# Performance work log

Hardware: AMD Instinct MI355X
Metric: run time of the kernel (lower is better)

## Reference

```python
import jax, jax.numpy as jnp
import numpy as np
from jax import lax

FEAT_X, FEAT_Y = 50, 37          # generate_anchors(50, 37)
BASE_SIZE, DSR = 8.0, 16.0
A = FEAT_X * FEAT_Y * 9          # 16650 anchors


def generate_anchors():
    # Vectorized version of the triple python loop; order: x, y, size, [b1,b2,b3]
    xs = jnp.arange(FEAT_X, dtype=jnp.float32)[:, None, None]
    ys = jnp.arange(FEAT_Y, dtype=jnp.float32)[None, :, None]
    s = jnp.array([BASE_SIZE, 2 * BASE_SIZE, 4 * BASE_SIZE], jnp.float32)[None, None, :]

    def box(x1, y1, x2, y2):
        return jnp.stack(jnp.broadcast_arrays(x1 * DSR, y1 * DSR, x2 * DSR, y2 * DSR), axis=-1)

    b1 = box(xs - s / 2, ys - s / 2, xs + s / 2, ys + s / 2)      # square
    b2 = box(xs - s,     ys - s / 4, xs + s,     ys + s / 4)      # wide
    b3 = box(xs - s / 4, ys - s,     xs + s / 4, ys + s)          # tall
    anchors = jnp.stack([b1, b2, b3], axis=3)  # (50,37,3 sizes,3 variants,4)
    return anchors.reshape(-1, 4)              # (16650,4)


def conv2d(x, w, b, padding):
    y = lax.conv_general_dilated(x, w, (1, 1), padding,
                                 dimension_numbers=("NCHW", "OIHW", "NCHW"))
    return y + b[None, :, None, None]


def pairwise_iou(anchors, gt):
    # anchors: (A,4), gt: (B,G,4) -> iou (B,A,G); zero when no positive overlap
    a = anchors[None, :, None, :]
    g = gt[:, None, :, :]
    area_a = (a[..., 2] - a[..., 0]) * (a[..., 3] - a[..., 1])
    area_g = (g[..., 2] - g[..., 0]) * (g[..., 3] - g[..., 1])
    left = jnp.maximum(a[..., 0], g[..., 0])
    right = jnp.minimum(a[..., 2], g[..., 2])
    top = jnp.maximum(a[..., 1], g[..., 1])
    bot = jnp.minimum(a[..., 3], g[..., 3])
    no_ov = (left >= right) | (top >= bot)
    inter = jnp.where(no_ov, 0.0, (right - left) * (bot - top))
    return jnp.where(no_ov, 0.0, inter / (area_a + area_g - inter))


def setup_inputs() -> dict:
    key = jax.random.key(0)
    k1, k2, k3, k4, k5, k6, k7, k8 = jax.random.split(key, 8)
    B, G = 8, 20
    feats = jax.random.normal(k1, (B, 512, FEAT_Y, FEAT_X), jnp.float32)
    # well-formed gt boxes inside an ~800x592 image
    raw = jax.random.uniform(k2, (B, G, 2, 2)) * jnp.array([800.0, 592.0])
    x1y1 = jnp.min(raw, axis=2)
    x2y2 = jnp.max(raw, axis=2) + 1.0
    gt_boxes = jnp.concatenate([x1y1, x2y2], axis=-1)  # (B,G,4)
    im_info = jnp.array([[592.0, 800.0, 1.0]], jnp.float32)  # (h, w, scale)
    s = 0.02
    w3 = jax.random.normal(k3, (512, 512, 3, 3), jnp.float32) * s
    b3 = jnp.zeros((512,), jnp.float32)
    wc = jax.random.normal(k4, (18, 512, 1, 1), jnp.float32) * s
    bc = jnp.zeros((18,), jnp.float32)
    wb = jax.random.normal(k5, (36, 512, 1, 1), jnp.float32) * s
    bb = jnp.zeros((36,), jnp.float32)
    return {"feats": feats, "w3": w3, "b3": b3, "wc": wc, "bc": bc,
            "wb": wb, "bb": bb, "gt_boxes": gt_boxes, "im_info": im_info}


def reference(feats, w3, b3, wc, bc, wb, bb, gt_boxes, im_info):
    B = feats.shape[0]
    anchors = generate_anchors()
    rpn_conv1 = jax.nn.relu(conv2d(feats, w3, b3, ((1, 1), (1, 1))))
    rpn_cls_score = conv2d(rpn_conv1, wc, bc, ((0, 0), (0, 0)))  # (B,18,H,W)
    Bc, C, H, W = rpn_cls_score.shape
    score_rs = rpn_cls_score.reshape(Bc, 2, (C * H) // 2, W)      # reshape(x, 2)
    rpn_cls_prob = jax.nn.softmax(score_rs, axis=1).reshape(Bc, 18, H, W)
    rpn_bbox_pred = conv2d(rpn_conv1, wb, bb, ((0, 0), (0, 0)))   # (B,36,H,W)

    # anchor-target assignment (training branch), faithful to original logic
    inside = ((anchors[:, 0] >= 0) & (anchors[:, 1] >= 0) &
              (anchors[:, 2] < im_info[0, 1]) & (anchors[:, 3] < im_info[0, 0]))
    iou = pairwise_iou(anchors, gt_boxes)                 # (B,A,G)
    iou = jnp.where(inside[None, :, None], iou, 0.0)      # outside anchors skipped
    G = gt_boxes.shape[1]
    # original: idxs = argmax(iou_matrix[:][j]) with j == last gt index
    idx = jnp.argmax(iou[:, G - 1, :], axis=-1)           # (B,)
    labels = jnp.zeros((B, anchors.shape[0]), jnp.float32)
    labels = labels.at[jnp.arange(B), idx].set(1.0)
    max_iou = jnp.max(iou, axis=-1)                       # (B,A)
    labels = jnp.where(inside[None, :] & (max_iou > 0.7), 0.0, labels)

    out = jnp.concatenate([rpn_cls_prob, rpn_bbox_pred], axis=1)  # (B,54,H,W)
    return out, iou, labels
```

## Files before the change

### kernel.cpp

```cpp
#include <hip/hip_runtime.h>

typedef unsigned short u16;
typedef unsigned int u32;
typedef float f32x4 __attribute__((ext_vector_type(4)));
typedef short bf16x8 __attribute__((ext_vector_type(8)));

#define NB 8
#define FH 37
#define FW 50
#define FHW 1850
#define MTOT 14800
#define CIN 512
#define KTOT 4608
#define HP 39
#define WP 52
#define ANCH 16650
#define NG 20
#define MPAD 14848
#define PSTRIDE 7602176

#define ZB 356
#define WTB 512
#define WHB 128
#define TRB 7424
#define PRE_TOT (ZB + WTB + WHB + TRB)

#define CONVB 1856
#define IOB 528

__device__ __forceinline__ u16 f2bf(float f) {
    u32 u = __float_as_uint(f);
    u += 0x7fffu + ((u >> 16) & 1u);
    return (u16)(u >> 16);
}

__device__ __forceinline__ void gl2lds16(const u16* g, u16* l) {
    __builtin_amdgcn_global_load_lds((const __attribute__((address_space(1))) void*)(g),
                                     (__attribute__((address_space(3))) void*)(l),
                                     16, 0, 0);
}

__device__ __forceinline__ void anchor_box(int a, float& x1, float& y1, float& x2, float& y2) {
    int x = a / 333;
    int rem = a - x * 333;
    int y = rem / 9;
    int r2 = rem - y * 9;
    int si = r2 / 3;
    int bi = r2 - si * 3;
    float s = (float)(8 << si);
    float fx = (float)x, fy = (float)y;
    float ax1, ay1, ax2, ay2;
    if (bi == 0)      { float h = s * 0.5f;  ax1 = fx - h; ay1 = fy - h; ax2 = fx + h; ay2 = fy + h; }
    else if (bi == 1) { float q = s * 0.25f; ax1 = fx - s; ay1 = fy - q; ax2 = fx + s; ay2 = fy + q; }
    else              { float q = s * 0.25f; ax1 = fx - q; ay1 = fy - s; ax2 = fx + q; ay2 = fy + s; }
    x1 = ax1 * 16.f; y1 = ay1 * 16.f; x2 = ax2 * 16.f; y2 = ay2 * 16.f;
}

__global__ __launch_bounds__(256) void k_pre(u16* __restrict__ apad,
                                             const float* __restrict__ w3, u16* __restrict__ wt,
                                             const float* __restrict__ wc, const float* __restrict__ wb,
                                             u16* __restrict__ whd,
                                             const float* __restrict__ feats) {
    __shared__ __attribute__((aligned(16))) char smraw[18432];
    int blk = blockIdx.x;
    int t = threadIdx.x;

    if (blk < ZB) {
        uint4* apad4 = (uint4*)apad;
        int i = blk * 256 + t;
        int img = i / 11392;
        int r = i - img * 11392;
        int u4;
        if (r < 3328) u4 = r;
        else if (r < 6656) u4 = 126464 + (r - 3328);
        else {
            int rp = r - 6656;
            int h = 1 + (rp >> 7);
            int c2 = rp & 127;
            int col = (c2 & 64) ? 51 : 0;
            u4 = (h * 52 + col) * 64 + (c2 & 63);
        }
        apad4[img * 129792 + u4] = make_uint4(0u, 0u, 0u, 0u);
    } else if (blk < ZB + WTB) {
        float* lt = (float*)smraw;
        int n = blk - ZB;
        const float* src = w3 + n * KTOT;
        for (int i = t; i < KTOT; i += 256) lt[i] = src[i];
        __syncthreads();
        u16* dst = wt + n * KTOT;
        for (int o = t; o < KTOT; o += 256) {
            int tap = o >> 9, ci = o & 511;
            dst[o] = f2bf(lt[ci * 9 + tap]);
        }
    } else if (blk < ZB + WTB + WHB) {
        int i = (blk - ZB - WTB) * 256 + t;
        int n = i >> 9;
        int ci = i & 511;
        float v = 0.f;
        if (n < 18) v = wc[n * 512 + ci];
        else if (n < 54) v = wb[(n - 18) * 512 + ci];
        whd[i] = f2bf(v);
    } else {
        float* tile = (float*)smraw;
        int q = blk - ZB - WTB - WHB;
        int xt = q % 58;
        int r2 = q / 58;
        int ct = r2 & 15;
        int img = r2 >> 4;
        int hw0 = xt * 32, c0 = ct * 32;
        int tx = t & 31, ty4 = t >> 5;
        #pragma unroll
        for (int rr = 0; rr < 4; rr++) {
            int ty = ty4 + rr * 8;
            int hw = hw0 + tx;
            if (hw < FHW) tile[ty * 33 + tx] = feats[(img * 512 + c0 + ty) * FHW + hw];
        }
        __syncthreads();
        #pragma unroll
        for (int rr = 0; rr < 4; rr++) {
            int ty = ty4 + rr * 8;
            int hw2 = hw0 + ty;
            if (hw2 < FHW) {
                int h = hw2 / FW, w = hw2 - h * FW;
                apad[(((img * HP) + h + 1) * WP + (w + 1)) * 512 + c0 + tx] = f2bf(tile[tx * 33 + ty]);
            }
        }
    }
}

__global__ __launch_bounds__(256) void k_conv(const u16* __restrict__ apad,
                                              const u16* __restrict__ wt,
                                              float* __restrict__ P,
                                              const float* __restrict__ gt,
                                              const float* __restrict__ im,
                                              float* __restrict__ iou_out,
                                              float* __restrict__ lab) {
    __shared__ __attribute__((aligned(16))) char sm[24576];
    __shared__ int idxs;
    int L = blockIdx.x;
    int tid = threadIdx.x;

    if (L < CONVB) {
        u16* As = (u16*)sm;
        u16* Bs = (u16*)(sm + 16384);
        int g = L >> 6;
        int pair = (L & 7) + 8 * g;
        int nb = (L >> 3) & 7;
        int mb = pair >> 1;
        int kh = pair & 1;
        int wave = tid >> 6, lane = tid & 63;
        int m0 = mb * 128;
        int n0 = nb * 64;
        int wr = wave >> 1, wn = wave & 1;
        int lm = lane & 15, lq = lane >> 4;
        int l7 = lm & 7;

        f32x4 acc[4][2] = {};

        int rloc = tid >> 3;
        int cg = (tid & 7) ^ (rloc & 7);
        int aBase[4], bBase[2];
        for (int i = 0; i < 4; i++) {
            int m = m0 + i * 32 + rloc; if (m > MTOT - 1) m = MTOT - 1;
            int b = m / FHW; int hw = m - b * FHW;
            int h = hw / FW; int w = hw - h * FW;
            aBase[i] = ((b * HP + h) * WP + w) * 512 + cg * 8;
        }
        for (int j = 0; j < 2; j++)
            bBase[j] = (n0 + j * 32 + rloc) * KTOT + cg * 8;

        u16* aL[4]; u16* bL[2];
        for (int i = 0; i < 4; i++) aL[i] = &As[(i * 32 + wave * 8) * 64];
        for (int j = 0; j < 2; j++) bL[j] = &Bs[(j * 32 + wave * 8) * 64];

        int kEnd = (kh + 1) * 2304;
        for (int kk = kh * 2304; kk < kEnd; kk += 64) {
            int tap = kk >> 9;
            int ci0 = kk & 511;
            int dy = tap / 3, dx = tap - dy * 3;
            int aOfs = (dy * WP + dx) * 512 + ci0;
            gl2lds16(apad + aBase[0] + aOfs, aL[0]);
            gl2lds16(apad + aBase[1] + aOfs, aL[1]);
            gl2lds16(apad + aBase[2] + aOfs, aL[2]);
            gl2lds16(apad + aBase[3] + aOfs, aL[3]);
            gl2lds16(wt + bBase[0] + kk, bL[0]);
            gl2lds16(wt + bBase[1] + kk, bL[1]);
            __syncthreads();
            bf16x8 a[2][4], b[2][2];
            #pragma unroll
            for (int ks = 0; ks < 2; ks++) {
                int slotb = ((ks * 4 + lq) ^ l7) * 8;
                #pragma unroll
                for (int i = 0; i < 4; i++)
                    a[ks][i] = *(const bf16x8*)&As[(wr * 64 + i * 16 + lm) * 64 + slotb];
                #pragma unroll
                for (int j = 0; j < 2; j++)
                    b[ks][j] = *(const bf16x8*)&Bs[(wn * 32 + j * 16 + lm) * 64 + slotb];
            }
            #pragma unroll
            for (int ks = 0; ks < 2; ks++)
                #pragma unroll
                for (int i = 0; i < 4; i++)
                    #pragma unroll
                    for (int j = 0; j < 2; j++)
                        acc[i][j] = __builtin_amdgcn_mfma_f32_16x16x32_bf16(a[ks][i], b[ks][j], acc[i][j], 0, 0, 0);
            __syncthreads();
        }

        float* Pp = P + (size_t)kh * PSTRIDE;
        for (int j = 0; j < 2; j++) {
            int n = n0 + wn * 32 + j * 16 + lm;
            for (int i = 0; i < 4; i++) {
                int mb2 = m0 + wr * 64 + i * 16 + lq * 4;
                for (int r = 0; r < 4; r++) {
                    int m = mb2 + r;
                    if (m < MTOT) Pp[m * 512 + n] = acc[i][j][r];
                }
            }
        }
    } else {
        float* g4 = (float*)sm;
        float* imv = g4 + 80;
        float* buf = g4 + 84;
        int q = L - CONVB;
        int at = q % 66;
        int b = q / 66;
        int t = tid;
        if (t < NG * 4) g4[t] = gt[b * NG * 4 + t];
        if (t < 2) imv[t] = im[t];
        __syncthreads();
        if (t == 0) {
            float x1, y1, x2, y2;
            anchor_box(19, x1, y1, x2, y2);
            bool inside = (x1 >= 0.f) && (y1 >= 0.f) && (x2 < imv[1]) && (y2 < imv[0]);
            float aa = (x2 - x1) * (y2 - y1);
            float best = -1.f; int bg = 0;
            for (int g2 = 0; g2 < NG; g2++) {
                float gx1 = g4[g2 * 4], gy1 = g4[g2 * 4 + 1], gx2 = g4[g2 * 4 + 2], gy2 = g4[g2 * 4 + 3];
                float l = fmaxf(x1, gx1), r = fminf(x2, gx2);
                float tp = fmaxf(y1, gy1), bo = fminf(y2, gy2);
                float v = 0.f;
                if (l < r && tp < bo) {
                    float inter = (r - l) * (bo - tp);
                    float ag = (gx2 - gx1) * (gy2 - gy1);
                    v = inter / (aa + ag - inter);
                }
                if (!inside) v = 0.f;
                if (v > best) { best = v; bg = g2; }
            }
            idxs = bg;
        }
        int a0 = at * 256;
        int a = a0 + t;
        float mx = 0.f;
        bool inside = false;
        if (a < ANCH) {
            float x1, y1, x2, y2;
            anchor_box(a, x1, y1, x2, y2);
            inside = (x1 >= 0.f) && (y1 >= 0.f) && (x2 < imv[1]) && (y2 < imv[0]);
            float aa = (x2 - x1) * (y2 - y1);
            for (int g2 = 0; g2 < NG; g2++) {
                float gx1 = g4[g2 * 4], gy1 = g4[g2 * 4 + 1], gx2 = g4[g2 * 4 + 2], gy2 = g4[g2 * 4 + 3];
                float l = fmaxf(x1, gx1), r = fminf(x2, gx2);
                float tp = fmaxf(y1, gy1), bo = fminf(y2, gy2);
                float v = 0.f;
                if (l < r && tp < bo) {
                    float inter = (r - l) * (bo - tp);
                    float ag = (gx2 - gx1) * (gy2 - gy1);
                    v = inter / (aa + ag - inter);
                }
                if (!inside) v = 0.f;
                buf[t * NG + g2] = v;
                mx = fmaxf(mx, v);
            }
        }
        __syncthreads();
        int rem = ANCH - a0;
        int cnt = (rem < 256 ? rem : 256) * NG;
        float* dst = iou_out + (b * ANCH + a0) * NG;
        for (int i = t; i < cnt; i += 256) dst[i] = buf[i];
        if (a < ANCH) {
            float lv = (a == idxs) ? 1.f : 0.f;
            if (inside && mx > 0.7f) lv = 0.f;
            lab[b * ANCH + a] = lv;
        }
    }
}

__global__ __launch_bounds__(256) void k_post(const float* __restrict__ P,
                                              const u16* __restrict__ whd,
                                              const float* __restrict__ b3,
                                              const float* __restrict__ bc,
                                              const float* __restrict__ bb,
                                              float* __restrict__ out) {
    __shared__ __attribute__((aligned(16))) u16 actT[32 * 64 * 8];
    __shared__ float Sl[4][16][68];
    int t = threadIdx.x;
    int m0 = blockIdx.x * 32;
    const float* P0 = P;
    const float* P1 = P + PSTRIDE;

    #pragma unroll
    for (int i = 0; i < 16; i++) {
        int idx = t + i * 256;
        int row = idx >> 7, col4 = idx & 127;
        size_t off = (size_t)(m0 + row) * 512 + col4 * 4;
        f32x4 p0 = *(const f32x4*)&P0[off];
        f32x4 p1 = *(const f32x4*)&P1[off];
        f32x4 bi = *(const f32x4*)&b3[col4 * 4];
        u32 lo, hi;
        {
            float v0 = p0[0] + p1[0] + bi[0]; v0 = v0 > 0.f ? v0 : 0.f;
            float v1 = p0[1] + p1[1] + bi[1]; v1 = v1 > 0.f ? v1 : 0.f;
            float v2 = p0[2] + p1[2] + bi[2]; v2 = v2 > 0.f ? v2 : 0.f;
            float v3 = p0[3] + p1[3] + bi[3]; v3 = v3 > 0.f ? v3 : 0.f;
            lo = (u32)f2bf(v0) | ((u32)f2bf(v1) << 16);
            hi = (u32)f2bf(v2) | ((u32)f2bf(v3) << 16);
        }
        int slot = row * 64 + ((col4 >> 1) ^ (row & 7));
        *(uint2*)&actT[slot * 8 + (col4 & 1) * 4] = make_uint2(lo, hi);
    }
    __syncthreads();

    int wave = t >> 6, lane = t & 63, lm = lane & 15, lq = lane >> 4;
    int g = wave >> 1, kh = wave & 1;
    int rowLoc = g * 16 + lm;
    f32x4 acc[4] = {};
    #pragma unroll
    for (int s = 0; s < 8; s++) {
        int kk = kh * 256 + s * 32;
        int c = (kk >> 3) + lq;
        bf16x8 a = *(const bf16x8*)&actT[(rowLoc * 64 + (c ^ (rowLoc & 7))) * 8];
        #pragma unroll
        for (int j = 0; j < 4; j++) {
            bf16x8 b = *(const bf16x8*)&whd[(j * 16 + lm) * 512 + kk + lq * 8];
            acc[j] = __builtin_amdgcn_mfma_f32_16x16x32_bf16(a, b, acc[j], 0, 0, 0);
        }
    }
    #pragma unroll
    for (int r = 0; r < 4; r++)
        #pragma unroll
        for (int j = 0; j < 4; j++)
            Sl[wave][lq * 4 + r][j * 16 + lm] = acc[j][r];
    __syncthreads();

    for (int i = t; i < 32 * 54; i += 256) {
        int row = i & 31, cc = i >> 5;
        int m = m0 + row;
        if (m >= MTOT) continue;
        int g2 = (row >> 4) * 2, rl = row & 15;
        float v;
        if (cc < 18) {
            int c0 = cc < 9 ? cc : cc - 9;
            float s0 = Sl[g2][rl][c0] + Sl[g2 + 1][rl][c0] + bc[c0];
            float s1 = Sl[g2][rl][c0 + 9] + Sl[g2 + 1][rl][c0 + 9] + bc[c0 + 9];
            float mx = fmaxf(s0, s1);
            float e0 = __expf(s0 - mx), e1 = __expf(s1 - mx);
            v = (cc < 9 ? e0 : e1) / (e0 + e1);
        } else {
            v = Sl[g2][rl][cc] + Sl[g2 + 1][rl][cc] + bb[cc - 18];
        }
        int b = m / FHW, hw = m - b * FHW;
        out[(b * 54 + cc) * FHW + hw] = v;
    }
}

extern "C" void kernel_launch(void* const* d_in, const int* in_sizes, int n_in,
                              void* d_out, int out_size, void* d_ws, size_t ws_size,
                              hipStream_t stream) {
    (void)in_sizes; (void)n_in; (void)out_size; (void)ws_size;
    const float* feats = (const float*)d_in[0];
    const float* w3    = (const float*)d_in[1];
    const float* b3    = (const float*)d_in[2];
    const float* wc    = (const float*)d_in[3];
    const float* bc    = (const float*)d_in[4];
    const float* wb    = (const float*)d_in[5];
    const float* bb    = (const float*)d_in[6];
    const float* gt    = (const float*)d_in[7];
    const float* im    = (const float*)d_in[8];
    float* out = (float*)d_out;
    char* ws = (char*)d_ws;

    u16* apad = (u16*)(ws);
    u16* wt   = (u16*)(ws + 16613376);
    u16* whd  = (u16*)(ws + 21331968);
    float* P  = (float*)(ws + 21397504);

    float* iou_out = out + 799200;
    float* lab     = out + 3463200;

    k_pre<<<dim3(PRE_TOT), dim3(256), 0, stream>>>(apad, w3, wt, wc, wb, whd, feats);
    k_conv<<<dim3(CONVB + IOB), dim3(256), 0, stream>>>(apad, wt, P, gt, im, iou_out, lab);
    k_post<<<dim3(464), dim3(256), 0, stream>>>(P, whd, b3, bc, bb, out);
}
```

Before: 206.8 us.

## Drop split-K and fuse bias/ReLU/heads into conv via last-block atomic counter

The 3x3 conv no longer splits K into two halves with fp32 partial outputs. Each block runs the full K loop and writes bias+ReLU activations directly as bf16. A per-M-tile atomic counter lets the last of the 8 N-blocks compute the 1x1 cls/bbox heads and softmax inline, which removes the separate post kernel and the fp32 partial round trip. The cost is half as many conv blocks, each with a longer serial K loop, so less parallelism. The tail work is also serialized on one block per M tile, and correctness depends on fences and the counter reset done in k_pre.

After: 367.7 us. +77.8%, slower.

```diff
diff --git a/kernel.cpp b/kernel.cpp
--- a/kernel.cpp
+++ b/kernel.cpp
@@ -16,8 +16,6 @@
 #define WP 52
 #define ANCH 16650
 #define NG 20
-#define MPAD 14848
-#define PSTRIDE 7602176
 
 #define ZB 356
 #define WTB 512
@@ -25,7 +23,7 @@
 #define TRB 7424
 #define PRE_TOT (ZB + WTB + WHB + TRB)
 
-#define CONVB 1856
+#define CONVB 960
 #define IOB 528
 
 __device__ __forceinline__ u16 f2bf(float f) {
@@ -60,7 +58,8 @@
                                              const float* __restrict__ w3, u16* __restrict__ wt,
                                              const float* __restrict__ wc, const float* __restrict__ wb,
                                              u16* __restrict__ whd,
-                                             const float* __restrict__ feats) {
+                                             const float* __restrict__ feats,
+                                             int* __restrict__ cnt) {
     __shared__ __attribute__((aligned(16))) char smraw[18432];
     int blk = blockIdx.x;
     int t = threadIdx.x;
@@ -100,7 +99,7 @@
         if (n < 18) v = wc[n * 512 + ci];
         else if (n < 54) v = wb[(n - 18) * 512 + ci];
         whd[i] = f2bf(v);
-    } else {
+    } else if (blk < PRE_TOT) {
         float* tile = (float*)smraw;
         int q = blk - ZB - WTB - WHB;
         int xt = q % 58;
@@ -125,29 +124,36 @@
                 apad[(((img * HP) + h + 1) * WP + (w + 1)) * 512 + c0 + tx] = f2bf(tile[tx * 33 + ty]);
             }
         }
+    } else {
+        if (t < 116) cnt[t] = 0;
     }
 }
 
 __global__ __launch_bounds__(256) void k_conv(const u16* __restrict__ apad,
                                               const u16* __restrict__ wt,
-                                              float* __restrict__ P,
+                                              const float* __restrict__ b3,
+                                              const float* __restrict__ bc,
+                                              const float* __restrict__ bb,
+                                              const u16* __restrict__ whd,
+                                              u16* __restrict__ act,
+                                              int* __restrict__ cnt,
                                               const float* __restrict__ gt,
                                               const float* __restrict__ im,
                                               float* __restrict__ iou_out,
-                                              float* __restrict__ lab) {
-    __shared__ __attribute__((aligned(16))) char sm[24576];
+                                              float* __restrict__ lab,
+                                              float* __restrict__ out) {
+    __shared__ __attribute__((aligned(16))) char sm[33280];
     __shared__ int idxs;
+    __shared__ int flagv;
     int L = blockIdx.x;
     int tid = threadIdx.x;
 
     if (L < CONVB) {
         u16* As = (u16*)sm;
         u16* Bs = (u16*)(sm + 16384);
-        int g = L >> 6;
-        int pair = (L & 7) + 8 * g;
+        int mb = (L & 7) + 8 * (L >> 6);
         int nb = (L >> 3) & 7;
-        int mb = pair >> 1;
-        int kh = pair & 1;
+        if (mb >= 116) return;
         int wave = tid >> 6, lane = tid & 63;
         int m0 = mb * 128;
         int n0 = nb * 64;
@@ -173,8 +179,7 @@
         for (int i = 0; i < 4; i++) aL[i] = &As[(i * 32 + wave * 8) * 64];
         for (int j = 0; j < 2; j++) bL[j] = &Bs[(j * 32 + wave * 8) * 64];
 
-        int kEnd = (kh + 1) * 2304;
-        for (int kk = kh * 2304; kk < kEnd; kk += 64) {
+        for (int kk = 0; kk < KTOT; kk += 64) {
             int tap = kk >> 9;
             int ci0 = kk & 511;
             int dy = tap / 3, dx = tap - dy * 3;
@@ -207,16 +212,81 @@
             __syncthreads();
         }
 
-        float* Pp = P + (size_t)kh * PSTRIDE;
         for (int j = 0; j < 2; j++) {
             int n = n0 + wn * 32 + j * 16 + lm;
+            float bias = b3[n];
             for (int i = 0; i < 4; i++) {
                 int mb2 = m0 + wr * 64 + i * 16 + lq * 4;
                 for (int r = 0; r < 4; r++) {
                     int m = mb2 + r;
-                    if (m < MTOT) Pp[m * 512 + n] = acc[i][j][r];
+                    if (m < MTOT) {
+                        float v = acc[i][j][r] + bias;
+                        act[m * 512 + n] = f2bf(v > 0.f ? v : 0.f);
+                    }
                 }
             }
+        }
+
+        __syncthreads();
+        __threadfence();
+        if (tid == 0) {
+            int old = __hip_atomic_fetch_add(&cnt[mb], 1, __ATOMIC_ACQ_REL,
+                                             __HIP_MEMORY_SCOPE_AGENT);
+            flagv = (old == 7);
+        }
+        __syncthreads();
+        if (!flagv) return;
+        __threadfence();
+
+        float* Sl2 = (float*)sm;
+        f32x4 acc2[2][4] = {};
+        int r0 = wave * 32;
+        int arow[2];
+        for (int i = 0; i < 2; i++) {
+            int m = m0 + r0 + i * 16 + lm; if (m > MTOT - 1) m = MTOT - 1;
+            arow[i] = m * 512;
+        }
+        for (int kk = 0; kk < 512; kk += 32) {
+            bf16x8 a[2], b[4];
+            #pragma unroll
+            for (int i = 0; i < 2; i++)
+                a[i] = *(const bf16x8*)&act[arow[i] + kk + lq * 8];
+            #pragma unroll
+            for (int j = 0; j < 4; j++)
+                b[j] = *(const bf16x8*)&whd[(j * 16 + lm) * 512 + kk + lq * 8];
+            #pragma unroll
+            for (int i = 0; i < 2; i++)
+                #pragma unroll
+                for (int j = 0; j < 4; j++)
+                    acc2[i][j] = __builtin_amdgcn_mfma_f32_16x16x32_bf16(a[i], b[j], acc2[i][j], 0, 0, 0);
+        }
+        #pragma unroll
+        for (int i = 0; i < 2; i++)
+            #pragma unroll
+            for (int r = 0; r < 4; r++)
+                #pragma unroll
+                for (int j = 0; j < 4; j++)
+                    Sl2[(r0 + i * 16 + lq * 4 + r) * 65 + j * 16 + lm] = acc2[i][j][r];
+        __syncthreads();
+
+        for (int i = tid; i < 54 * 128; i += 256) {
+            int cc = i >> 7, row = i & 127;
+            int m = m0 + row;
+            if (m >= MTOT) continue;
+            const float* Sr = &Sl2[row * 65];
+            float v;
+            if (cc < 18) {
+                int c0 = cc < 9 ? cc : cc - 9;
+                float s0 = Sr[c0] + bc[c0];
+                float s1 = Sr[c0 + 9] + bc[c0 + 9];
+                float mx = fmaxf(s0, s1);
+                float e0 = __expf(s0 - mx), e1 = __expf(s1 - mx);
+                v = (cc < 9 ? e0 : e1) / (e0 + e1);
+            } else {
+                v = Sr[cc] + bb[cc - 18];
+            }
+            int b = m / FHW, hw = m - b * FHW;
+            out[(b * 54 + cc) * FHW + hw] = v;
         }
     } else {
         float* g4 = (float*)sm;
@@ -276,92 +346,14 @@
         }
         __syncthreads();
         int rem = ANCH - a0;
-        int cnt = (rem < 256 ? rem : 256) * NG;
+        int cnt2 = (rem < 256 ? rem : 256) * NG;
         float* dst = iou_out + (b * ANCH + a0) * NG;
-        for (int i = t; i < cnt; i += 256) dst[i] = buf[i];
+        for (int i = t; i < cnt2; i += 256) dst[i] = buf[i];
         if (a < ANCH) {
             float lv = (a == idxs) ? 1.f : 0.f;
             if (inside && mx > 0.7f) lv = 0.f;
             lab[b * ANCH + a] = lv;
         }
-    }
-}
-
-__global__ __launch_bounds__(256) void k_post(const float* __restrict__ P,
-                                              const u16* __restrict__ whd,
-                                              const float* __restrict__ b3,
-                                              const float* __restrict__ bc,
-                                              const float* __restrict__ bb,
-                                              float* __restrict__ out) {
-    __shared__ __attribute__((aligned(16))) u16 actT[32 * 64 * 8];
-    __shared__ float Sl[4][16][68];
-    int t = threadIdx.x;
-    int m0 = blockIdx.x * 32;
-    const float* P0 = P;
-    const float* P1 = P + PSTRIDE;
-
-    #pragma unroll
-    for (int i = 0; i < 16; i++) {
-        int idx = t + i * 256;
-        int row = idx >> 7, col4 = idx & 127;
-        size_t off = (size_t)(m0 + row) * 512 + col4 * 4;
-        f32x4 p0 = *(const f32x4*)&P0[off];
-        f32x4 p1 = *(const f32x4*)&P1[off];
-        f32x4 bi = *(const f32x4*)&b3[col4 * 4];
-        u32 lo, hi;
-        {
-            float v0 = p0[0] + p1[0] + bi[0]; v0 = v0 > 0.f ? v0 : 0.f;
-            float v1 = p0[1] + p1[1] + bi[1]; v1 = v1 > 0.f ? v1 : 0.f;
-            float v2 = p0[2] + p1[2] + bi[2]; v2 = v2 > 0.f ? v2 : 0.f;
-            float v3 = p0[3] + p1[3] + bi[3]; v3 = v3 > 0.f ? v3 : 0.f;
-            lo = (u32)f2bf(v0) | ((u32)f2bf(v1) << 16);
-            hi = (u32)f2bf(v2) | ((u32)f2bf(v3) << 16);
-        }
-        int slot = row * 64 + ((col4 >> 1) ^ (row & 7));
-        *(uint2*)&actT[slot * 8 + (col4 & 1) * 4] = make_uint2(lo, hi);
-    }
-    __syncthreads();
-
-    int wave = t >> 6, lane = t & 63, lm = lane & 15, lq = lane >> 4;
-    int g = wave >> 1, kh = wave & 1;
-    int rowLoc = g * 16 + lm;
-    f32x4 acc[4] = {};
-    #pragma unroll
-    for (int s = 0; s < 8; s++) {
-        int kk = kh * 256 + s * 32;
-        int c = (kk >> 3) + lq;
-        bf16x8 a = *(const bf16x8*)&actT[(rowLoc * 64 + (c ^ (rowLoc & 7))) * 8];
-        #pragma unroll
-        for (int j = 0; j < 4; j++) {
-            bf16x8 b = *(const bf16x8*)&whd[(j * 16 + lm) * 512 + kk + lq * 8];
-            acc[j] = __builtin_amdgcn_mfma_f32_16x16x32_bf16(a, b, acc[j], 0, 0, 0);
-        }
-    }
-    #pragma unroll
-    for (int r = 0; r < 4; r++)
-        #pragma unroll
-        for (int j = 0; j < 4; j++)
-            Sl[wave][lq * 4 + r][j * 16 + lm] = acc[j][r];
-    __syncthreads();
-
-    for (int i = t; i < 32 * 54; i += 256) {
-        int row = i & 31, cc = i >> 5;
-        int m = m0 + row;
-        if (m >= MTOT) continue;
-        int g2 = (row >> 4) * 2, rl = row & 15;
-        float v;
-        if (cc < 18) {
-            int c0 = cc < 9 ? cc : cc - 9;
-            float s0 = Sl[g2][rl][c0] + Sl[g2 + 1][rl][c0] + bc[c0];
-            float s1 = Sl[g2][rl][c0 + 9] + Sl[g2 + 1][rl][c0 + 9] + bc[c0 + 9];
-            float mx = fmaxf(s0, s1);
-            float e0 = __expf(s0 - mx), e1 = __expf(s1 - mx);
-            v = (cc < 9 ? e0 : e1) / (e0 + e1);
-        } else {
-            v = Sl[g2][rl][cc] + Sl[g2 + 1][rl][cc] + bb[cc - 18];
-        }
-        int b = m / FHW, hw = m - b * FHW;
-        out[(b * 54 + cc) * FHW + hw] = v;
     }
 }
 
@@ -384,12 +376,13 @@
     u16* apad = (u16*)(ws);
     u16* wt   = (u16*)(ws + 16613376);
     u16* whd  = (u16*)(ws + 21331968);
-    float* P  = (float*)(ws + 21397504);
+    u16* act  = (u16*)(ws + 21397504);
+    int* cnt  = (int*)(ws + 36552704);
 
     float* iou_out = out + 799200;
     float* lab     = out + 3463200;
 
-    k_pre<<<dim3(PRE_TOT), dim3(256), 0, stream>>>(apad, w3, wt, wc, wb, whd, feats);
-    k_conv<<<dim3(CONVB + IOB), dim3(256), 0, stream>>>(apad, wt, P, gt, im, iou_out, lab);
-    k_post<<<dim3(464), dim3(256), 0, stream>>>(P, whd, b3, bc, bb, out);
-}
+    k_pre<<<dim3(PRE_TOT + 1), dim3(256), 0, stream>>>(apad, w3, wt, wc, wb, whd, feats, cnt);
+    k_conv<<<dim3(CONVB + IOB), dim3(256), 0, stream>>>(apad, wt, b3, bc, bb, whd, act, cnt,
+                                                        gt, im, iou_out, lab, out);
+}
```
